# Kernel optimization log

Hardware: AMD Instinct MI355X
Metric: run time of the kernel (lower is better)

## Reference

```python
import jax, jax.numpy as jnp
import numpy as np

REG_M = 0.1     # reg_m_bregman
N_ITER = 30     # fixed MM iteration count (POT uses numItermax=1000 w/ early stop)
EPS = 1e-16     # POT's stabilizer added to the denominator


def setup_inputs() -> dict:
    key = jax.random.key(0)
    kx, ky = jax.random.split(key)
    x = jax.random.normal(kx, (4096, 256), dtype=jnp.float32)
    y = jax.random.normal(ky, (4096, 256), dtype=jnp.float32)
    # L2-normalize embeddings so squared distances lie in [0,4] and the
    # KL kernel exp(-M / (2*reg_m)) stays in a representable range.
    x = x / jnp.linalg.norm(x, axis=1, keepdims=True)
    y = y / jnp.linalg.norm(y, axis=1, keepdims=True)
    return {"x": x, "y": y}


def reference(x, y):
    m, n = x.shape[0], y.shape[0]
    # ot.dist default metric: squared euclidean  M[i,j] = ||x_i - y_j||^2
    M = (jnp.sum(x * x, axis=1)[:, None]
         + jnp.sum(y * y, axis=1)[None, :]
         - 2.0 * (x @ y.T))                                  # [m, n]
    a = jnp.full((m,), 1.0 / m, dtype=x.dtype)
    b = jnp.full((n,), 1.0 / n, dtype=x.dtype)
    # POT mm_unbalanced, div='kl', reg_m1=reg_m2=reg_m, reg=0:
    # r1 = r2 = 1/2, K = sqrt(a_i b_j) * exp(-M / (2*reg_m)), G0 = a (x) b,
    # G <- K * G / (sqrt(rowsum_i) * sqrt(colsum_j) + eps)
    K = jnp.sqrt(a[:, None] * b[None, :]) * jnp.exp(-M / (2.0 * REG_M))
    G0 = a[:, None] * b[None, :]

    def step(G, _):
        Gd = jnp.sqrt(G.sum(axis=1)[:, None] * G.sum(axis=0)[None, :]) + EPS
        return K * G / Gd, None

    Pi, _ = jax.lax.scan(step, G0, None, length=N_ITER)
    # (Pi @ M.T).mean() = sum_j (sum_i Pi[i,j]) * (sum_k M[k,j]) / m^2
    return jnp.dot(Pi.sum(axis=0), M.sum(axis=0)) / (m * m)
```

## Files before the change

### kernel.cpp

```cpp
#include <hip/hip_runtime.h>
#include <math.h>

#define MDIM 4096
#define NDIM 4096
#define DDIM 256
#define N_ITER 30

#define TWO_KAPPA 14.426950408889634
#define CLCONST  (-12.0 - TWO_KAPPA)

__device__ __forceinline__ unsigned encf(float f) {
  unsigned u = __float_as_uint(f);
  return (u & 0x80000000u) ? ~u : (u | 0x80000000u);
}
__device__ __forceinline__ float decf(unsigned u) {
  return __uint_as_float((u & 0x80000000u) ? (u ^ 0x80000000u) : ~u);
}

__global__ void norms_kernel(const float* __restrict__ x, const float* __restrict__ y,
                             float* __restrict__ xx, float* __restrict__ yy,
                             float* __restrict__ Sxx) {
  int wid = threadIdx.x >> 6, lane = threadIdx.x & 63;
  int row = blockIdx.x * 4 + wid;
  const float* src = (row < MDIM) ? x : y;
  int r = (row < MDIM) ? row : row - MDIM;
  const float4* p = (const float4*)(src + (size_t)r * DDIM);
  float4 v = p[lane];
  float s = v.x*v.x + v.y*v.y + v.z*v.z + v.w*v.w;
  #pragma unroll
  for (int off = 32; off; off >>= 1) s += __shfl_down(s, off);
  if (lane == 0) {
    if (row < MDIM) { xx[r] = s; atomicAdd(Sxx, s); }
    else            { yy[r] = s; }
  }
}

__global__ void sx_kernel(const float* __restrict__ x, float* __restrict__ sx) {
  int tx = threadIdx.x;
  int r0 = blockIdx.x * 16;
  float s = 0.f;
  #pragma unroll
  for (int r = 0; r < 16; ++r) s += x[(size_t)(r0 + r) * DDIM + tx];
  atomicAdd(&sx[tx], s);
}

__global__ void colM_kernel(const float* __restrict__ y, const float* __restrict__ sx,
                            const float* __restrict__ yy, const float* __restrict__ Sxx,
                            float* __restrict__ colM) {
  int wid = threadIdx.x >> 6, lane = threadIdx.x & 63;
  int j = blockIdx.x * 4 + wid;
  const float4* py = (const float4*)(y + (size_t)j * DDIM);
  const float4* ps = (const float4*)sx;
  float4 a = py[lane], b = ps[lane];
  float s = a.x*b.x + a.y*b.y + a.z*b.z + a.w*b.w;
  #pragma unroll
  for (int off = 32; off; off >>= 1) s += __shfl_down(s, off);
  if (lane == 0) colM[j] = *Sxx + (float)MDIM * yy[j] - 2.f * s;
}

#define BMT 128
#define BKT 32
#define APAD 132
__global__ __launch_bounds__(256)
void gemm_d_kernel(const float* __restrict__ x, const float* __restrict__ y,
                   short* __restrict__ D16, float* __restrict__ maxdot) {
  __shared__ float As[BKT][APAD];
  __shared__ float Bs[BKT][APAD];
  int tid = threadIdx.x;
  int bm = blockIdx.x & 31, bn = blockIdx.x >> 5;
  int tx = tid & 15, ty = tid >> 4;
  float acc[8][8] = {};
  for (int k0 = 0; k0 < DDIM; k0 += BKT) {
    #pragma unroll
    for (int q = 0; q < 4; ++q) {
      int li = tid + 256 * q;
      int row = li >> 3, ks = (li & 7) * 4;
      float4 v = *(const float4*)(x + (size_t)(bm * BMT + row) * DDIM + k0 + ks);
      As[ks+0][row] = v.x; As[ks+1][row] = v.y; As[ks+2][row] = v.z; As[ks+3][row] = v.w;
    }
    #pragma unroll
    for (int q = 0; q < 4; ++q) {
      int li = tid + 256 * q;
      int row = li >> 3, ks = (li & 7) * 4;
      float4 v = *(const float4*)(y + (size_t)(bn * BMT + row) * DDIM + k0 + ks);
      Bs[ks+0][row] = v.x; Bs[ks+1][row] = v.y; Bs[ks+2][row] = v.z; Bs[ks+3][row] = v.w;
    }
    __syncthreads();
    #pragma unroll
    for (int kk = 0; kk < BKT; ++kk) {
      float a[8], b[8];
      float4 a0 = *(const float4*)&As[kk][ty*8];
      float4 a1 = *(const float4*)&As[kk][ty*8+4];
      a[0]=a0.x; a[1]=a0.y; a[2]=a0.z; a[3]=a0.w; a[4]=a1.x; a[5]=a1.y; a[6]=a1.z; a[7]=a1.w;
      #pragma unroll
      for (int cg = 0; cg < 4; ++cg) {
        float2 bv = *(const float2*)&Bs[kk][2*tx + 32*cg];
        b[2*cg] = bv.x; b[2*cg+1] = bv.y;
      }
      #pragma unroll
      for (int r = 0; r < 8; ++r)
        #pragma unroll
        for (int c = 0; c < 8; ++c) acc[r][c] = fmaf(a[r], b[c], acc[r][c]);
    }
    __syncthreads();
  }
  float tmax = -1.f;
  #pragma unroll
  for (int r = 0; r < 8; ++r) {
    int row = bm*BMT + ty*8 + r;
    #pragma unroll
    for (int cg = 0; cg < 4; ++cg) {
      float d0 = acc[r][2*cg], d1 = acc[r][2*cg+1];
      tmax = fmaxf(tmax, fmaxf(d0, d1));
      int lo = __float2int_rn(fminf(fmaxf(d0 * 65536.f, -32767.f), 32767.f));
      int hi = __float2int_rn(fminf(fmaxf(d1 * 65536.f, -32767.f), 32767.f));
      int iv = (lo & 0xFFFF) | (hi << 16);
      int col = bn*BMT + 2*tx + 32*cg;
      *(int*)(D16 + (size_t)row * NDIM + col) = iv;
    }
  }
  __shared__ float sm[4];
  #pragma unroll
  for (int off = 32; off; off >>= 1) tmax = fmaxf(tmax, __shfl_down(tmax, off));
  int lane = tid & 63, wid = tid >> 6;
  if (lane == 0) sm[wid] = tmax;
  __syncthreads();
  if (tid == 0) {
    float m = fmaxf(fmaxf(sm[0], sm[1]), fmaxf(sm[2], sm[3]));
    atomicMax((int*)maxdot, __float_as_int(fmaxf(m, 0.f)));
  }
}

#define IR 16
template<int MODE>
__global__ __launch_bounds__(1024)
void iter_kernel(const short* __restrict__ D16,
                 const float* __restrict__ phi_in, float* __restrict__ phi_out,
                 const float* __restrict__ psi_in,
                 float* __restrict__ partial,
                 const float* __restrict__ maxdot,
                 const unsigned* __restrict__ psimaxU,
                 unsigned* __restrict__ phimaxU,
                 int t, float sD, float tCL, float s2k) {
  __shared__ float rp[IR][17];
  int tid = threadIdx.x;
  int lane = tid & 63, wid = tid >> 6;
  int row0 = blockIdx.x * IR;
  int j0 = tid * 4;

  float tLmax = fmaf(s2k, maxdot[0], tCL);
  float psimax, phimax, p0, p1, p2, p3;
  if constexpr (MODE == 0) {
    psimax = -6.f; phimax = -6.f;
    p0 = p1 = p2 = p3 = -6.f;
  } else {
    psimax = decf(psimaxU[t]);
    phimax = decf(phimaxU[t]);
    float4 pv = *(const float4*)(psi_in + j0);
    p0 = pv.x; p1 = pv.y; p2 = pv.z; p3 = pv.w;
  }
  float Sr = tLmax + psimax - 100.f;
  float Sc = tLmax + phimax - 100.f;
  float W  = tCL - Sr;
  float Wc = tCL - Sc;
  float P0 = p0 + W, P1 = p1 + W, P2 = p2 + W, P3 = p3 + W;

  float c0 = 0.f, c1 = 0.f, c2 = 0.f, c3 = 0.f;
  #pragma unroll 4
  for (int r = 0; r < IR; ++r) {
    int row = row0 + r;
    float phi_row = (MODE == 0) ? -6.f : phi_in[row];
    float Crow = Wc + phi_row;
    int2 dv = *(const int2*)(D16 + (size_t)row * NDIM + j0);
    float d0 = (float)((short)(dv.x & 0xFFFF));
    float d1 = (float)(dv.x >> 16);
    float d2 = (float)((short)(dv.y & 0xFFFF));
    float d3 = (float)(dv.y >> 16);
    c0 += exp2f(fmaf(d0, sD, Crow));
    c1 += exp2f(fmaf(d1, sD, Crow));
    c2 += exp2f(fmaf(d2, sD, Crow));
    c3 += exp2f(fmaf(d3, sD, Crow));
    float racc = exp2f(fmaf(d0, sD, P0)) + exp2f(fmaf(d1, sD, P1))
               + exp2f(fmaf(d2, sD, P2)) + exp2f(fmaf(d3, sD, P3));
    #pragma unroll
    for (int off = 32; off; off >>= 1) racc += __shfl_down(racc, off);
    if (lane == 0) rp[r][wid] = racc;
  }
  __syncthreads();
  if (tid < IR) {
    float s = 0.f;
    #pragma unroll
    for (int w = 0; w < 16; ++w) s += rp[tid][w];
    int row = row0 + tid;
    float phi_row = (MODE == 0) ? -6.f : phi_in[row];
    float pn = 0.5f * (phi_row - Sr - log2f(fmaxf(s, 1e-30f)));
    phi_out[row] = pn;
    #pragma unroll
    for (int off = 8; off; off >>= 1) pn = fmaxf(pn, __shfl_down(pn, off));
    if (tid == 0) atomicMax(&phimaxU[t + 1], encf(pn));
  }
  *(float4*)(partial + (size_t)blockIdx.x * NDIM + j0) = make_float4(c0, c1, c2, c3);
}

template<int FIRST>
__global__ __launch_bounds__(1024)
void finish_kernel(const float* __restrict__ partial,
                   const float* __restrict__ psi_in, float* __restrict__ psi_out,
                   float* __restrict__ ct,
                   const float* __restrict__ maxdot,
                   unsigned* __restrict__ psimaxU,
                   const unsigned* __restrict__ phimaxU,
                   int t, float prevCL, float prev_s2k) {
  __shared__ float red[8][132];
  __shared__ float sm[2];
  int tid = threadIdx.x;
  int jloc = tid & 127, c = tid >> 7;
  int j = blockIdx.x * 128 + jloc;
  float s = 0.f;
  #pragma unroll
  for (int k = 0; k < 32; ++k)
    s += partial[(size_t)(c * 32 + k) * NDIM + j];
  red[c][jloc] = s;
  __syncthreads();
  if (tid < 128) {
    float tot = red[0][jloc];
    #pragma unroll
    for (int cc = 1; cc < 8; ++cc) tot += red[cc][jloc];
    float tLmax_prev = fmaf(prev_s2k, maxdot[0], prevCL);
    float phimax_prev = FIRST ? -6.f : decf(phimaxU[t - 1]);
    float Sc_prev = tLmax_prev + phimax_prev - 100.f;
    float psi_prev = FIRST ? -6.f : psi_in[j];
    float pn = 0.5f * (psi_prev - Sc_prev - log2f(fmaxf(tot, 1e-30f)));
    psi_out[j] = pn;
    ct[j] = tot;
    int lane = tid & 63;
    #pragma unroll
    for (int off = 32; off; off >>= 1) pn = fmaxf(pn, __shfl_down(pn, off));
    if (lane == 0) sm[tid >> 6] = pn;
  }
  __syncthreads();
  if (tid == 0) atomicMax(&psimaxU[t], encf(fmaxf(sm[0], sm[1])));
}

__global__ __launch_bounds__(1024)
void loss_kernel(const float* __restrict__ ct, const float* __restrict__ psi30,
                 const float* __restrict__ colM,
                 const float* __restrict__ maxdot, const unsigned* __restrict__ phimaxU,
                 float* __restrict__ out, float lastCL, float last_s2k) {
  __shared__ float sp[16];
  int tid = threadIdx.x, lane = tid & 63, wid = tid >> 6;
  int j0 = tid * 4;
  float tLmax = fmaf(last_s2k, maxdot[0], lastCL);
  float Sc30 = tLmax + decf(phimaxU[N_ITER]) - 100.f;
  float4 cv = *(const float4*)(ct + j0);
  float4 pv = *(const float4*)(psi30 + j0);
  float4 mv = *(const float4*)(colM + j0);
  float s = exp2f(log2f(fmaxf(cv.x, 1e-30f)) + pv.x + Sc30 + log2f(mv.x))
          + exp2f(log2f(fmaxf(cv.y, 1e-30f)) + pv.y + Sc30 + log2f(mv.y))
          + exp2f(log2f(fmaxf(cv.z, 1e-30f)) + pv.z + Sc30 + log2f(mv.z))
          + exp2f(log2f(fmaxf(cv.w, 1e-30f)) + pv.w + Sc30 + log2f(mv.w));
  #pragma unroll
  for (int off = 32; off; off >>= 1) s += __shfl_down(s, off);
  if (lane == 0) sp[wid] = s;
  __syncthreads();
  if (tid == 0) {
    float tot = 0.f;
    #pragma unroll
    for (int w = 0; w < 16; ++w) tot += sp[w];
    out[0] = tot * (1.f / ((float)MDIM * (float)MDIM));
  }
}

extern "C" void kernel_launch(void* const* d_in, const int* in_sizes, int n_in,
                              void* d_out, int out_size, void* d_ws, size_t ws_size,
                              hipStream_t stream) {
  const float* x = (const float*)d_in[0];
  const float* y = (const float*)d_in[1];
  float* out = (float*)d_out;

  char* ws = (char*)d_ws;
  size_t off = 0;
  auto alloc = [&](size_t bytes) -> void* {
    void* p = ws + off;
    off += (bytes + 255) & ~(size_t)255;
    return p;
  };
  short*    D16     = (short*)alloc((size_t)MDIM * NDIM * 2);
  float*    partial = (float*)alloc((size_t)256 * NDIM * 4);
  float*    xx      = (float*)alloc(MDIM * 4);
  float*    yy      = (float*)alloc(NDIM * 4);
  float*    sx      = (float*)alloc(DDIM * 4);
  float*    colM    = (float*)alloc(NDIM * 4);
  float*    Sxx     = (float*)alloc(4);
  float*    maxd    = (float*)alloc(4);
  unsigned* psimaxU = (unsigned*)alloc(64 * 4);
  unsigned* phimaxU = (unsigned*)alloc(64 * 4);
  float*    psi     = (float*)alloc(NDIM * 4);
  float*    psidmy  = (float*)alloc(NDIM * 4);
  float*    ct      = (float*)alloc(NDIM * 4);
  float*    phib[2];
  phib[0] = (float*)alloc(MDIM * 4); phib[1] = (float*)alloc(MDIM * 4);

  hipMemsetAsync(Sxx, 0, 4, stream);
  hipMemsetAsync(maxd, 0, 4, stream);
  hipMemsetAsync(sx, 0, DDIM * 4, stream);
  hipMemsetAsync(psimaxU, 0, 64 * 4, stream);
  hipMemsetAsync(phimaxU, 0, 64 * 4, stream);

  norms_kernel<<<2048, 256, 0, stream>>>(x, y, xx, yy, Sxx);
  sx_kernel<<<256, 256, 0, stream>>>(x, sx);
  colM_kernel<<<1024, 256, 0, stream>>>(y, sx, yy, Sxx, colM);
  gemm_d_kernel<<<1024, 256, 0, stream>>>(x, y, D16, maxd);

  {
    int t = 1;
    float sD  = (float)((double)t * TWO_KAPPA / 65536.0);
    float tCL = (float)((double)t * CLCONST);
    float s2k = (float)((double)t * TWO_KAPPA);
    iter_kernel<0><<<256, 1024, 0, stream>>>(D16, phib[1], phib[0], psi, partial,
                                             maxd, psimaxU, phimaxU, t, sD, tCL, s2k);
  }
  for (int t = 2; t <= N_ITER; ++t) {
    float prevCL  = (float)((double)(t - 1) * CLCONST);
    float prev2k  = (float)((double)(t - 1) * TWO_KAPPA);
    if (t == 2)
      finish_kernel<1><<<32, 1024, 0, stream>>>(partial, psi, psi, ct, maxd,
                                                psimaxU, phimaxU, t, prevCL, prev2k);
    else
      finish_kernel<0><<<32, 1024, 0, stream>>>(partial, psi, psi, ct, maxd,
                                                psimaxU, phimaxU, t, prevCL, prev2k);
    float sD  = (float)((double)t * TWO_KAPPA / 65536.0);
    float tCL = (float)((double)t * CLCONST);
    float s2k = (float)((double)t * TWO_KAPPA);
    iter_kernel<1><<<256, 1024, 0, stream>>>(D16, phib[t & 1], phib[(t + 1) & 1], psi,
                                             partial, maxd, psimaxU, phimaxU,
                                             t, sD, tCL, s2k);
  }
  {
    float prevCL = (float)((double)N_ITER * CLCONST);
    float prev2k = (float)((double)N_ITER * TWO_KAPPA);
    finish_kernel<0><<<32, 1024, 0, stream>>>(partial, psi, psidmy, ct, maxd,
                                              psimaxU, phimaxU, N_ITER + 1, prevCL, prev2k);
    loss_kernel<<<1, 1024, 0, stream>>>(ct, psi, colM, maxd, phimaxU, out, prevCL, prev2k);
  }
}
```

Measured before the change: 851.5 us.

## Use split-bf16 MFMA GEMM and fuse iterations into one cooperative persistent kernel

Replaces the scalar FP32 distance GEMM with a bf16 hi/lo split (three MFMA products per tile) fed by a new conversion kernel. It also merges the 30 pairs of iter and finish launches and the loss kernel into one cooperative kernel that uses grid-wide syncs between phases. The aim is to cut GEMM compute time and the overhead of about 60 kernel launches. The split-bf16 product loses some precision compared with FP32, and grid syncs add their own latency.

Measured after the change: 2.275 ms. 167% more time.

```diff
diff --git a/kernel.cpp b/kernel.cpp
--- a/kernel.cpp
+++ b/kernel.cpp
@@ -1,5 +1,8 @@
 #include <hip/hip_runtime.h>
+#include <hip/hip_cooperative_groups.h>
 #include <math.h>
+
+namespace cg = cooperative_groups;
 
 #define MDIM 4096
 #define NDIM 4096
@@ -9,6 +12,9 @@
 #define TWO_KAPPA 14.426950408889634
 #define CLCONST  (-12.0 - TWO_KAPPA)
 
+typedef __attribute__((ext_vector_type(8))) short bf16x8;
+typedef __attribute__((ext_vector_type(4))) float f32x4;
+
 __device__ __forceinline__ unsigned encf(float f) {
   unsigned u = __float_as_uint(f);
   return (u & 0x80000000u) ? ~u : (u | 0x80000000u);
@@ -16,6 +22,8 @@
 __device__ __forceinline__ float decf(unsigned u) {
   return __uint_as_float((u & 0x80000000u) ? (u ^ 0x80000000u) : ~u);
 }
+__device__ __forceinline__ unsigned ldvu(const unsigned* p) { return *(const volatile unsigned*)p; }
+__device__ __forceinline__ float    ldvf(const float* p)    { return *(const volatile float*)p; }
 
 __global__ void norms_kernel(const float* __restrict__ x, const float* __restrict__ y,
                              float* __restrict__ xx, float* __restrict__ yy,
@@ -58,71 +66,100 @@
   if (lane == 0) colM[j] = *Sxx + (float)MDIM * yy[j] - 2.f * s;
 }
 
-#define BMT 128
-#define BKT 32
-#define APAD 132
+__global__ void split_kernel(const float* __restrict__ x, const float* __restrict__ y,
+                             ushort* __restrict__ xh, ushort* __restrict__ xl,
+                             ushort* __restrict__ yh, ushort* __restrict__ yl) {
+  int g = blockIdx.x * 256 + threadIdx.x;
+  int e; const float4* src; ushort* dh; ushort* dl;
+  if (g < 262144) { e = g;          src = (const float4*)x; dh = xh; dl = xl; }
+  else            { e = g - 262144; src = (const float4*)y; dh = yh; dl = yl; }
+  float4 v = src[e];
+  float f[4] = {v.x, v.y, v.z, v.w};
+  ushort hs[4], ls[4];
+  #pragma unroll
+  for (int i = 0; i < 4; ++i) {
+    unsigned u = __float_as_uint(f[i]);
+    unsigned hr = (u + 0x7FFFu + ((u >> 16) & 1u)) >> 16;
+    hs[i] = (ushort)hr;
+    float hf = __uint_as_float(hr << 16);
+    float lo = f[i] - hf;
+    unsigned ul = __float_as_uint(lo);
+    unsigned lr = (ul + 0x7FFFu + ((ul >> 16) & 1u)) >> 16;
+    ls[i] = (ushort)lr;
+  }
+  *(ushort4*)(dh + (size_t)e * 4) = make_ushort4(hs[0], hs[1], hs[2], hs[3]);
+  *(ushort4*)(dl + (size_t)e * 4) = make_ushort4(ls[0], ls[1], ls[2], ls[3]);
+}
+
+#define GPAD 56
 __global__ __launch_bounds__(256)
-void gemm_d_kernel(const float* __restrict__ x, const float* __restrict__ y,
-                   short* __restrict__ D16, float* __restrict__ maxdot) {
-  __shared__ float As[BKT][APAD];
-  __shared__ float Bs[BKT][APAD];
+void gemm_mfma_kernel(const ushort* __restrict__ xh, const ushort* __restrict__ xl,
+                      const ushort* __restrict__ yh, const ushort* __restrict__ yl,
+                      short* __restrict__ D16, float* __restrict__ maxdot) {
+  __shared__ ushort As[2][128][GPAD];
+  __shared__ ushort Bs[2][128][GPAD];
   int tid = threadIdx.x;
+  int lane = tid & 63, wid = tid >> 6;
   int bm = blockIdx.x & 31, bn = blockIdx.x >> 5;
-  int tx = tid & 15, ty = tid >> 4;
-  float acc[8][8] = {};
-  for (int k0 = 0; k0 < DDIM; k0 += BKT) {
+  int wrow = (wid >> 1) * 64, wcol = (wid & 1) * 64;
+  f32x4 acc[4][4] = {};
+
+  int c0 = tid, c1 = tid + 256;
+  int r0 = c0 >> 2, k80 = (c0 & 3) * 8;
+  int r1 = c1 >> 2, k81 = (c1 & 3) * 8;
+  const size_t arow0 = (size_t)(bm * 128 + r0) * DDIM;
+  const size_t arow1 = (size_t)(bm * 128 + r1) * DDIM;
+  const size_t brow0 = (size_t)(bn * 128 + r0) * DDIM;
+  const size_t brow1 = (size_t)(bn * 128 + r1) * DDIM;
+
+  for (int k0 = 0; k0 < DDIM; k0 += 32) {
+    *(uint4*)&As[0][r0][k80] = *(const uint4*)(xh + arow0 + k0 + k80);
+    *(uint4*)&As[0][r1][k81] = *(const uint4*)(xh + arow1 + k0 + k81);
+    *(uint4*)&As[1][r0][k80] = *(const uint4*)(xl + arow0 + k0 + k80);
+    *(uint4*)&As[1][r1][k81] = *(const uint4*)(xl + arow1 + k0 + k81);
+    *(uint4*)&Bs[0][r0][k80] = *(const uint4*)(yh + brow0 + k0 + k80);
+    *(uint4*)&Bs[0][r1][k81] = *(const uint4*)(yh + brow1 + k0 + k81);
+    *(uint4*)&Bs[1][r0][k80] = *(const uint4*)(yl + brow0 + k0 + k80);
+    *(uint4*)&Bs[1][r1][k81] = *(const uint4*)(yl + brow1 + k0 + k81);
+    __syncthreads();
+    int fr = lane & 15, kg = lane >> 4;
+    bf16x8 ah[4], al[4], bh[4], bl[4];
     #pragma unroll
-    for (int q = 0; q < 4; ++q) {
-      int li = tid + 256 * q;
-      int row = li >> 3, ks = (li & 7) * 4;
-      float4 v = *(const float4*)(x + (size_t)(bm * BMT + row) * DDIM + k0 + ks);
-      As[ks+0][row] = v.x; As[ks+1][row] = v.y; As[ks+2][row] = v.z; As[ks+3][row] = v.w;
+    for (int i = 0; i < 4; ++i) {
+      ah[i] = *(const bf16x8*)&As[0][wrow + i * 16 + fr][kg * 8];
+      al[i] = *(const bf16x8*)&As[1][wrow + i * 16 + fr][kg * 8];
+      bh[i] = *(const bf16x8*)&Bs[0][wcol + i * 16 + fr][kg * 8];
+      bl[i] = *(const bf16x8*)&Bs[1][wcol + i * 16 + fr][kg * 8];
     }
     #pragma unroll
-    for (int q = 0; q < 4; ++q) {
-      int li = tid + 256 * q;
-      int row = li >> 3, ks = (li & 7) * 4;
-      float4 v = *(const float4*)(y + (size_t)(bn * BMT + row) * DDIM + k0 + ks);
-      Bs[ks+0][row] = v.x; Bs[ks+1][row] = v.y; Bs[ks+2][row] = v.z; Bs[ks+3][row] = v.w;
-    }
+    for (int i = 0; i < 4; ++i)
+      #pragma unroll
+      for (int j = 0; j < 4; ++j) {
+        acc[i][j] = __builtin_amdgcn_mfma_f32_16x16x32_bf16(ah[i], bh[j], acc[i][j], 0, 0, 0);
+        acc[i][j] = __builtin_amdgcn_mfma_f32_16x16x32_bf16(ah[i], bl[j], acc[i][j], 0, 0, 0);
+        acc[i][j] = __builtin_amdgcn_mfma_f32_16x16x32_bf16(al[i], bh[j], acc[i][j], 0, 0, 0);
+      }
     __syncthreads();
+  }
+  float tmax = -1.f;
+  #pragma unroll
+  for (int i = 0; i < 4; ++i) {
     #pragma unroll
-    for (int kk = 0; kk < BKT; ++kk) {
-      float a[8], b[8];
-      float4 a0 = *(const float4*)&As[kk][ty*8];
-      float4 a1 = *(const float4*)&As[kk][ty*8+4];
-      a[0]=a0.x; a[1]=a0.y; a[2]=a0.z; a[3]=a0.w; a[4]=a1.x; a[5]=a1.y; a[6]=a1.z; a[7]=a1.w;
-      #pragma unroll
-      for (int cg = 0; cg < 4; ++cg) {
-        float2 bv = *(const float2*)&Bs[kk][2*tx + 32*cg];
-        b[2*cg] = bv.x; b[2*cg+1] = bv.y;
+    for (int j = 0; j < 4; ++j) {
+      int col = bn * 128 + wcol + j * 16 + (lane & 15);
+      #pragma unroll
+      for (int r = 0; r < 4; ++r) {
+        float d = acc[i][j][r];
+        tmax = fmaxf(tmax, d);
+        int q = __float2int_rn(fminf(fmaxf(d * 65536.f, -32767.f), 32767.f));
+        int row = bm * 128 + wrow + i * 16 + (lane >> 4) * 4 + r;
+        D16[(size_t)row * NDIM + col] = (short)q;
       }
-      #pragma unroll
-      for (int r = 0; r < 8; ++r)
-        #pragma unroll
-        for (int c = 0; c < 8; ++c) acc[r][c] = fmaf(a[r], b[c], acc[r][c]);
-    }
-    __syncthreads();
-  }
-  float tmax = -1.f;
-  #pragma unroll
-  for (int r = 0; r < 8; ++r) {
-    int row = bm*BMT + ty*8 + r;
-    #pragma unroll
-    for (int cg = 0; cg < 4; ++cg) {
-      float d0 = acc[r][2*cg], d1 = acc[r][2*cg+1];
-      tmax = fmaxf(tmax, fmaxf(d0, d1));
-      int lo = __float2int_rn(fminf(fmaxf(d0 * 65536.f, -32767.f), 32767.f));
-      int hi = __float2int_rn(fminf(fmaxf(d1 * 65536.f, -32767.f), 32767.f));
-      int iv = (lo & 0xFFFF) | (hi << 16);
-      int col = bn*BMT + 2*tx + 32*cg;
-      *(int*)(D16 + (size_t)row * NDIM + col) = iv;
     }
   }
   __shared__ float sm[4];
   #pragma unroll
   for (int off = 32; off; off >>= 1) tmax = fmaxf(tmax, __shfl_down(tmax, off));
-  int lane = tid & 63, wid = tid >> 6;
   if (lane == 0) sm[wid] = tmax;
   __syncthreads();
   if (tid == 0) {
@@ -131,144 +168,114 @@
   }
 }
 
-#define IR 16
-template<int MODE>
 __global__ __launch_bounds__(1024)
-void iter_kernel(const short* __restrict__ D16,
-                 const float* __restrict__ phi_in, float* __restrict__ phi_out,
-                 const float* __restrict__ psi_in,
-                 float* __restrict__ partial,
-                 const float* __restrict__ maxdot,
-                 const unsigned* __restrict__ psimaxU,
-                 unsigned* __restrict__ phimaxU,
-                 int t, float sD, float tCL, float s2k) {
-  __shared__ float rp[IR][17];
-  int tid = threadIdx.x;
-  int lane = tid & 63, wid = tid >> 6;
-  int row0 = blockIdx.x * IR;
+void solve_kernel(const short* __restrict__ D16, float* __restrict__ partial,
+                  float* __restrict__ phi, float* __restrict__ psi,
+                  const float* __restrict__ maxdot,
+                  unsigned* psimaxU, unsigned* phimaxU,
+                  const float* __restrict__ colM,
+                  float* lossacc, float* __restrict__ out) {
+  cg::grid_group gg = cg::this_grid();
+  __shared__ float rp[16][17];
+  __shared__ float bred[16][17];
+  int tid = threadIdx.x, lane = tid & 63, wid = tid >> 6;
+  int blk = blockIdx.x;
+  int row0 = blk * 16;
   int j0 = tid * 4;
-
-  float tLmax = fmaf(s2k, maxdot[0], tCL);
-  float psimax, phimax, p0, p1, p2, p3;
-  if constexpr (MODE == 0) {
-    psimax = -6.f; phimax = -6.f;
-    p0 = p1 = p2 = p3 = -6.f;
-  } else {
-    psimax = decf(psimaxU[t]);
-    phimax = decf(phimaxU[t]);
-    float4 pv = *(const float4*)(psi_in + j0);
-    p0 = pv.x; p1 = pv.y; p2 = pv.z; p3 = pv.w;
-  }
-  float Sr = tLmax + psimax - 100.f;
-  float Sc = tLmax + phimax - 100.f;
-  float W  = tCL - Sr;
-  float Wc = tCL - Sc;
-  float P0 = p0 + W, P1 = p1 + W, P2 = p2 + W, P3 = p3 + W;
-
-  float c0 = 0.f, c1 = 0.f, c2 = 0.f, c3 = 0.f;
-  #pragma unroll 4
-  for (int r = 0; r < IR; ++r) {
-    int row = row0 + r;
-    float phi_row = (MODE == 0) ? -6.f : phi_in[row];
-    float Crow = Wc + phi_row;
-    int2 dv = *(const int2*)(D16 + (size_t)row * NDIM + j0);
-    float d0 = (float)((short)(dv.x & 0xFFFF));
-    float d1 = (float)(dv.x >> 16);
-    float d2 = (float)((short)(dv.y & 0xFFFF));
-    float d3 = (float)(dv.y >> 16);
-    c0 += exp2f(fmaf(d0, sD, Crow));
-    c1 += exp2f(fmaf(d1, sD, Crow));
-    c2 += exp2f(fmaf(d2, sD, Crow));
-    c3 += exp2f(fmaf(d3, sD, Crow));
-    float racc = exp2f(fmaf(d0, sD, P0)) + exp2f(fmaf(d1, sD, P1))
-               + exp2f(fmaf(d2, sD, P2)) + exp2f(fmaf(d3, sD, P3));
-    #pragma unroll
-    for (int off = 32; off; off >>= 1) racc += __shfl_down(racc, off);
-    if (lane == 0) rp[r][wid] = racc;
-  }
-  __syncthreads();
-  if (tid < IR) {
-    float s = 0.f;
-    #pragma unroll
-    for (int w = 0; w < 16; ++w) s += rp[tid][w];
-    int row = row0 + tid;
-    float phi_row = (MODE == 0) ? -6.f : phi_in[row];
-    float pn = 0.5f * (phi_row - Sr - log2f(fmaxf(s, 1e-30f)));
-    phi_out[row] = pn;
-    #pragma unroll
-    for (int off = 8; off; off >>= 1) pn = fmaxf(pn, __shfl_down(pn, off));
-    if (tid == 0) atomicMax(&phimaxU[t + 1], encf(pn));
-  }
-  *(float4*)(partial + (size_t)blockIdx.x * NDIM + j0) = make_float4(c0, c1, c2, c3);
-}
-
-template<int FIRST>
-__global__ __launch_bounds__(1024)
-void finish_kernel(const float* __restrict__ partial,
-                   const float* __restrict__ psi_in, float* __restrict__ psi_out,
-                   float* __restrict__ ct,
-                   const float* __restrict__ maxdot,
-                   unsigned* __restrict__ psimaxU,
-                   const unsigned* __restrict__ phimaxU,
-                   int t, float prevCL, float prev_s2k) {
-  __shared__ float red[8][132];
-  __shared__ float sm[2];
-  int tid = threadIdx.x;
-  int jloc = tid & 127, c = tid >> 7;
-  int j = blockIdx.x * 128 + jloc;
-  float s = 0.f;
-  #pragma unroll
-  for (int k = 0; k < 32; ++k)
-    s += partial[(size_t)(c * 32 + k) * NDIM + j];
-  red[c][jloc] = s;
-  __syncthreads();
-  if (tid < 128) {
-    float tot = red[0][jloc];
-    #pragma unroll
-    for (int cc = 1; cc < 8; ++cc) tot += red[cc][jloc];
-    float tLmax_prev = fmaf(prev_s2k, maxdot[0], prevCL);
-    float phimax_prev = FIRST ? -6.f : decf(phimaxU[t - 1]);
-    float Sc_prev = tLmax_prev + phimax_prev - 100.f;
-    float psi_prev = FIRST ? -6.f : psi_in[j];
-    float pn = 0.5f * (psi_prev - Sc_prev - log2f(fmaxf(tot, 1e-30f)));
-    psi_out[j] = pn;
-    ct[j] = tot;
-    int lane = tid & 63;
-    #pragma unroll
-    for (int off = 32; off; off >>= 1) pn = fmaxf(pn, __shfl_down(pn, off));
-    if (lane == 0) sm[tid >> 6] = pn;
-  }
-  __syncthreads();
-  if (tid == 0) atomicMax(&psimaxU[t], encf(fmaxf(sm[0], sm[1])));
-}
-
-__global__ __launch_bounds__(1024)
-void loss_kernel(const float* __restrict__ ct, const float* __restrict__ psi30,
-                 const float* __restrict__ colM,
-                 const float* __restrict__ maxdot, const unsigned* __restrict__ phimaxU,
-                 float* __restrict__ out, float lastCL, float last_s2k) {
-  __shared__ float sp[16];
-  int tid = threadIdx.x, lane = tid & 63, wid = tid >> 6;
-  int j0 = tid * 4;
-  float tLmax = fmaf(last_s2k, maxdot[0], lastCL);
-  float Sc30 = tLmax + decf(phimaxU[N_ITER]) - 100.f;
-  float4 cv = *(const float4*)(ct + j0);
-  float4 pv = *(const float4*)(psi30 + j0);
-  float4 mv = *(const float4*)(colM + j0);
-  float s = exp2f(log2f(fmaxf(cv.x, 1e-30f)) + pv.x + Sc30 + log2f(mv.x))
-          + exp2f(log2f(fmaxf(cv.y, 1e-30f)) + pv.y + Sc30 + log2f(mv.y))
-          + exp2f(log2f(fmaxf(cv.z, 1e-30f)) + pv.z + Sc30 + log2f(mv.z))
-          + exp2f(log2f(fmaxf(cv.w, 1e-30f)) + pv.w + Sc30 + log2f(mv.w));
-  #pragma unroll
-  for (int off = 32; off; off >>= 1) s += __shfl_down(s, off);
-  if (lane == 0) sp[wid] = s;
-  __syncthreads();
-  if (tid == 0) {
-    float tot = 0.f;
-    #pragma unroll
-    for (int w = 0; w < 16; ++w) tot += sp[w];
-    out[0] = tot * (1.f / ((float)MDIM * (float)MDIM));
-  }
+  float md = maxdot[0];
+
+  for (int t = 1; t <= N_ITER; ++t) {
+    float sD  = (float)((double)t * (TWO_KAPPA / 65536.0));
+    float tCL = (float)((double)t * CLCONST);
+    float s2k = (float)((double)t * TWO_KAPPA);
+    float tLmax = fmaf(s2k, md, tCL);
+    float psimax, phimax, p0, p1, p2, p3;
+    if (t == 1) { psimax = phimax = -6.f; p0 = p1 = p2 = p3 = -6.f; }
+    else {
+      psimax = decf(ldvu(&psimaxU[t]));
+      phimax = decf(ldvu(&phimaxU[t]));
+      float4 pv = *(const float4*)(psi + j0);
+      p0 = pv.x; p1 = pv.y; p2 = pv.z; p3 = pv.w;
+    }
+    float Sr = tLmax + psimax - 100.f;
+    float Sc = tLmax + phimax - 100.f;
+    float W  = tCL - Sr;
+    float Wc = tCL - Sc;
+    float P0 = p0 + W, P1 = p1 + W, P2 = p2 + W, P3 = p3 + W;
+
+    float c0 = 0.f, c1 = 0.f, c2 = 0.f, c3 = 0.f;
+    #pragma unroll 4
+    for (int r = 0; r < 16; ++r) {
+      int row = row0 + r;
+      float phi_row = (t == 1) ? -6.f : phi[row];
+      float Crow = Wc + phi_row;
+      int2 dv = *(const int2*)(D16 + (size_t)row * NDIM + j0);
+      float d0 = (float)((short)(dv.x & 0xFFFF));
+      float d1 = (float)(dv.x >> 16);
+      float d2 = (float)((short)(dv.y & 0xFFFF));
+      float d3 = (float)(dv.y >> 16);
+      c0 += exp2f(fmaf(d0, sD, Crow));
+      c1 += exp2f(fmaf(d1, sD, Crow));
+      c2 += exp2f(fmaf(d2, sD, Crow));
+      c3 += exp2f(fmaf(d3, sD, Crow));
+      float racc = exp2f(fmaf(d0, sD, P0)) + exp2f(fmaf(d1, sD, P1))
+                 + exp2f(fmaf(d2, sD, P2)) + exp2f(fmaf(d3, sD, P3));
+      #pragma unroll
+      for (int off = 32; off; off >>= 1) racc += __shfl_down(racc, off);
+      if (lane == 0) rp[r][wid] = racc;
+    }
+    __syncthreads();
+    if (tid < 16) {
+      float s = 0.f;
+      #pragma unroll
+      for (int w = 0; w < 16; ++w) s += rp[tid][w];
+      int row = row0 + tid;
+      float phi_row = (t == 1) ? -6.f : phi[row];
+      float pn = 0.5f * (phi_row - Sr - log2f(fmaxf(s, 1e-30f)));
+      phi[row] = pn;
+      #pragma unroll
+      for (int o = 8; o; o >>= 1) pn = fmaxf(pn, __shfl_down(pn, o));
+      if (tid == 0) atomicMax(&phimaxU[t + 1], encf(pn));
+    }
+    *(float4*)(partial + (size_t)blk * NDIM + j0) = make_float4(c0, c1, c2, c3);
+    gg.sync();
+
+    {
+      int cloc = tid & 15, bgrp = tid >> 4;
+      int j = blk * 16 + cloc;
+      float s = partial[(size_t)bgrp * NDIM + j]
+              + partial[(size_t)(bgrp + 64) * NDIM + j]
+              + partial[(size_t)(bgrp + 128) * NDIM + j]
+              + partial[(size_t)(bgrp + 192) * NDIM + j];
+      s += __shfl_xor(s, 16);
+      s += __shfl_xor(s, 32);
+      if (lane < 16) bred[wid][lane] = s;
+      __syncthreads();
+      if (tid < 16) {
+        float tot = bred[0][tid];
+        #pragma unroll
+        for (int w = 1; w < 16; ++w) tot += bred[w][tid];
+        int jj = blk * 16 + tid;
+        if (t < N_ITER) {
+          float psiv = (t == 1) ? -6.f : psi[jj];
+          float pn = 0.5f * (psiv - Sc - log2f(fmaxf(tot, 1e-30f)));
+          psi[jj] = pn;
+          #pragma unroll
+          for (int o = 8; o; o >>= 1) pn = fmaxf(pn, __shfl_down(pn, o));
+          if (tid == 0) atomicMax(&psimaxU[t + 1], encf(pn));
+        } else {
+          float contrib = exp2f(log2f(fmaxf(tot, 1e-30f)) + psi[jj] + Sc + log2f(colM[jj]));
+          #pragma unroll
+          for (int o = 8; o; o >>= 1) contrib += __shfl_down(contrib, o);
+          if (tid == 0) atomicAdd(lossacc, contrib);
+        }
+      }
+      __syncthreads();
+    }
+    gg.sync();
+  }
+  if (blk == 0 && tid == 0)
+    out[0] = ldvf(lossacc) * (1.f / ((float)MDIM * (float)MDIM));
 }
 
 extern "C" void kernel_launch(void* const* d_in, const int* in_sizes, int n_in,
@@ -287,6 +294,10 @@
   };
   short*    D16     = (short*)alloc((size_t)MDIM * NDIM * 2);
   float*    partial = (float*)alloc((size_t)256 * NDIM * 4);
+  ushort*   xh      = (ushort*)alloc((size_t)MDIM * DDIM * 2);
+  ushort*   xl      = (ushort*)alloc((size_t)MDIM * DDIM * 2);
+  ushort*   yh      = (ushort*)alloc((size_t)NDIM * DDIM * 2);
+  ushort*   yl      = (ushort*)alloc((size_t)NDIM * DDIM * 2);
   float*    xx      = (float*)alloc(MDIM * 4);
   float*    yy      = (float*)alloc(NDIM * 4);
   float*    sx      = (float*)alloc(DDIM * 4);
@@ -295,52 +306,26 @@
   float*    maxd    = (float*)alloc(4);
   unsigned* psimaxU = (unsigned*)alloc(64 * 4);
   unsigned* phimaxU = (unsigned*)alloc(64 * 4);
+  float*    phi     = (float*)alloc(MDIM * 4);
   float*    psi     = (float*)alloc(NDIM * 4);
-  float*    psidmy  = (float*)alloc(NDIM * 4);
-  float*    ct      = (float*)alloc(NDIM * 4);
-  float*    phib[2];
-  phib[0] = (float*)alloc(MDIM * 4); phib[1] = (float*)alloc(MDIM * 4);
+  float*    lossacc = (float*)alloc(4);
 
   hipMemsetAsync(Sxx, 0, 4, stream);
   hipMemsetAsync(maxd, 0, 4, stream);
   hipMemsetAsync(sx, 0, DDIM * 4, stream);
   hipMemsetAsync(psimaxU, 0, 64 * 4, stream);
   hipMemsetAsync(phimaxU, 0, 64 * 4, stream);
+  hipMemsetAsync(lossacc, 0, 4, stream);
 
   norms_kernel<<<2048, 256, 0, stream>>>(x, y, xx, yy, Sxx);
   sx_kernel<<<256, 256, 0, stream>>>(x, sx);
   colM_kernel<<<1024, 256, 0, stream>>>(y, sx, yy, Sxx, colM);
-  gemm_d_kernel<<<1024, 256, 0, stream>>>(x, y, D16, maxd);
-
-  {
-    int t = 1;
-    float sD  = (float)((double)t * TWO_KAPPA / 65536.0);
-    float tCL = (float)((double)t * CLCONST);
-    float s2k = (float)((double)t * TWO_KAPPA);
-    iter_kernel<0><<<256, 1024, 0, stream>>>(D16, phib[1], phib[0], psi, partial,
-                                             maxd, psimaxU, phimaxU, t, sD, tCL, s2k);
-  }
-  for (int t = 2; t <= N_ITER; ++t) {
-    float prevCL  = (float)((double)(t - 1) * CLCONST);
-    float prev2k  = (float)((double)(t - 1) * TWO_KAPPA);
-    if (t == 2)
-      finish_kernel<1><<<32, 1024, 0, stream>>>(partial, psi, psi, ct, maxd,
-                                                psimaxU, phimaxU, t, prevCL, prev2k);
-    else
-      finish_kernel<0><<<32, 1024, 0, stream>>>(partial, psi, psi, ct, maxd,
-                                                psimaxU, phimaxU, t, prevCL, prev2k);
-    float sD  = (float)((double)t * TWO_KAPPA / 65536.0);
-    float tCL = (float)((double)t * CLCONST);
-    float s2k = (float)((double)t * TWO_KAPPA);
-    iter_kernel<1><<<256, 1024, 0, stream>>>(D16, phib[t & 1], phib[(t + 1) & 1], psi,
-                                             partial, maxd, psimaxU, phimaxU,
-                                             t, sD, tCL, s2k);
-  }
-  {
-    float prevCL = (float)((double)N_ITER * CLCONST);
-    float prev2k = (float)((double)N_ITER * TWO_KAPPA);
-    finish_kernel<0><<<32, 1024, 0, stream>>>(partial, psi, psidmy, ct, maxd,
-                                              psimaxU, phimaxU, N_ITER + 1, prevCL, prev2k);
-    loss_kernel<<<1, 1024, 0, stream>>>(ct, psi, colM, maxd, phimaxU, out, prevCL, prev2k);
-  }
-}
+  split_kernel<<<2048, 256, 0, stream>>>(x, y, xh, xl, yh, yl);
+  gemm_mfma_kernel<<<1024, 256, 0, stream>>>(xh, xl, yh, yl, D16, maxd);
+
+  void* kargs[] = {(void*)&D16, (void*)&partial, (void*)&phi, (void*)&psi,
+                   (void*)&maxd, (void*)&psimaxU, (void*)&phimaxU,
+                   (void*)&colM, (void*)&lossacc, (void*)&out};
+  hipLaunchCooperativeKernel((void*)solve_kernel, dim3(256), dim3(1024),
+                             kargs, 0, stream);
+}
```
